# Optimization experiments

Measured on AMD Instinct MI355X. Metric: run time of the kernel, lower is better.

## Reference

```python
import jax, jax.numpy as jnp
import numpy as np

B, N, D = 4, 2048, 512
NUM_HEADS = 8
NUM_LAYERS = 2
HID_AW = D // NUM_HEADS  # 64, hidden/bottleneck of atten_weight MLP
LN_EPS = 1e-5


def _gelu(x):
    return jax.nn.gelu(x, approximate=False)


def _ln(x, g, b):
    m = jnp.mean(x, axis=-1, keepdims=True)
    v = jnp.var(x, axis=-1, keepdims=True)
    return (x - m) * jax.lax.rsqrt(v + LN_EPS) * g + b


def _mlp(x, params):
    # params: list of (W, b); gelu between layers, no act on the last layer
    for W, b in params[:-1]:
        x = _gelu(x @ W.T + b)
    W, b = params[-1]
    return x @ W.T + b


def _mha(x, valid, Wqkv, bqkv, Wo, bo):
    # x: [B, S, D], valid: [B, S] bool key mask (True = attend)
    Bx, S, Dm = x.shape
    Hd = Dm // NUM_HEADS
    qkv = x @ Wqkv.T + bqkv                      # [B, S, 3D]
    q, k, v = jnp.split(qkv, 3, axis=-1)
    def heads(t):
        return t.reshape(Bx, S, NUM_HEADS, Hd).transpose(0, 2, 1, 3)
    q, k, v = heads(q), heads(k), heads(v)       # [B, H, S, Hd]
    scores = jnp.einsum('bhqd,bhkd->bhqk', q, k) / jnp.sqrt(jnp.asarray(Hd, x.dtype))
    scores = jnp.where(valid[:, None, None, :], scores, jnp.asarray(-1e9, x.dtype))
    attn = jax.nn.softmax(scores, axis=-1)
    out = jnp.einsum('bhqk,bhkd->bhqd', attn, v).transpose(0, 2, 1, 3).reshape(Bx, S, Dm)
    return out @ Wo.T + bo


def _get_atten(emb, valid, cls_token, ln_g, ln_b, mha_params):
    # emb: [B, N, D] weighted instance embeddings; valid: [B, N] group membership
    Bx = emb.shape[0]
    seq = jnp.concatenate([jnp.broadcast_to(cls_token, (Bx, 1, D)), emb], axis=1)  # [B, N+1, D]
    mask = jnp.concatenate([jnp.ones((Bx, 1), bool), valid], axis=1)               # cls always valid
    z = _ln(seq, ln_g, ln_b)
    a = z
    for p in mha_params:
        a = _mha(a, mask, *p)
        a = _ln(z + a, ln_g, ln_b)
    return a[:, 0]  # cls embedding [B, D]


def setup_inputs() -> dict:
    key = jax.random.key(0)
    ks = jax.random.split(key, 32)
    i = iter(range(32))
    def w(shape, scale=0.02):
        return (jax.random.normal(ks[next(i)], shape, jnp.float32) * scale)
    inp = {}
    inp['x'] = jax.random.normal(ks[next(i)], (B, N, D), jnp.float32)
    inp['cls_token'] = w((1, D), 1.0)
    inp['ln_g'] = jnp.ones((D,), jnp.float32)
    inp['ln_b'] = jnp.zeros((D,), jnp.float32)
    # atten_weight MLP: D -> 64 -> 64 -> 1
    inp['aw_W0'] = w((HID_AW, D)); inp['aw_b0'] = jnp.zeros((HID_AW,), jnp.float32)
    inp['aw_W1'] = w((HID_AW, HID_AW)); inp['aw_b1'] = jnp.zeros((HID_AW,), jnp.float32)
    inp['aw_W2'] = w((1, HID_AW)); inp['aw_b2'] = jnp.zeros((1,), jnp.float32)
    # proj MLP: 2D -> D -> D -> D
    inp['pr_W0'] = w((D, 2 * D)); inp['pr_b0'] = jnp.zeros((D,), jnp.float32)
    inp['pr_W1'] = w((D, D)); inp['pr_b1'] = jnp.zeros((D,), jnp.float32)
    inp['pr_W2'] = w((D, D)); inp['pr_b2'] = jnp.zeros((D,), jnp.float32)
    # 2 shared MultiheadAttention layers
    inp['m0_Wqkv'] = w((3 * D, D)); inp['m0_bqkv'] = jnp.zeros((3 * D,), jnp.float32)
    inp['m0_Wo'] = w((D, D)); inp['m0_bo'] = jnp.zeros((D,), jnp.float32)
    inp['m1_Wqkv'] = w((3 * D, D)); inp['m1_bqkv'] = jnp.zeros((3 * D,), jnp.float32)
    inp['m1_Wo'] = w((D, D)); inp['m1_bo'] = jnp.zeros((D,), jnp.float32)
    return inp


def reference(x, cls_token, ln_g, ln_b,
              aw_W0, aw_b0, aw_W1, aw_b1, aw_W2, aw_b2,
              pr_W0, pr_b0, pr_W1, pr_b1, pr_W2, pr_b2,
              m0_Wqkv, m0_bqkv, m0_Wo, m0_bo,
              m1_Wqkv, m1_bqkv, m1_Wo, m1_bo):
    aw = [(aw_W0, aw_b0), (aw_W1, aw_b1), (aw_W2, aw_b2)]
    pr = [(pr_W0, pr_b0), (pr_W1, pr_b1), (pr_W2, pr_b2)]
    mha_params = [(m0_Wqkv, m0_bqkv, m0_Wo, m0_bo), (m1_Wqkv, m1_bqkv, m1_Wo, m1_bo)]
    # per-instance attention weights
    weight = jax.nn.sigmoid(_mlp(x, aw)[..., 0])       # [B, N]
    neg_mask = weight < 0.5
    pos_mask = jnp.logical_not(neg_mask)
    neg_emb = x * jnp.power(weight, 1.5)[..., None]    # w^(3/2)
    pos_emb = x * jnp.power(weight, 2.0 / 3.0)[..., None]  # w^(2/3)
    neg_cls = _get_atten(neg_emb, neg_mask, cls_token, ln_g, ln_b, mha_params)  # [B, D]
    pos_cls = _get_atten(pos_emb, pos_mask, cls_token, ln_g, ln_b, mha_params)  # [B, D]
    emb = jnp.concatenate([neg_cls, pos_cls], axis=-1)  # [B, 2D]
    return _mlp(emb, pr)                                # [B, D]
```

## Files before the change

kernel.cpp:

```cpp
#include <hip/hip_runtime.h>
#include <hip/hip_bf16.h>

#define B_SZ 4
#define N_INST 2048
#define D_MODEL 512
#define S_TOT 2049
#define NH 8
#define HD 64
#define VB 8
#define VROWS (VB*S_TOT)
#define NCHUNK 16

typedef __attribute__((ext_vector_type(4))) float f32x4;
typedef __attribute__((ext_vector_type(8))) short bf16x8;

__device__ __forceinline__ float gelu_exact(float x){ return 0.5f*x*(1.f+erff(x*0.70710678118654752f)); }
__device__ __forceinline__ unsigned short f2bf(float x){
  unsigned int u = __float_as_uint(x);
  u += 0x7fffu + ((u>>16)&1u);
  return (unsigned short)(u>>16);
}
__device__ __forceinline__ float bfval(unsigned short u){ return __uint_as_float(((unsigned int)u)<<16); }
__device__ __forceinline__ unsigned int pk2(unsigned short lo, unsigned short hi){
  return (unsigned int)lo | ((unsigned int)hi << 16);
}
__device__ __forceinline__ unsigned short ext16(unsigned int u, int hi){
  return (unsigned short)(hi ? (u>>16) : (u & 0xffffu));
}

#define GLOAD16(gp, lp) __builtin_amdgcn_global_load_lds( \
    (const __attribute__((address_space(1))) void*)(gp), \
    (__attribute__((address_space(3))) void*)(lp), 16, 0, 0)

__global__ __launch_bounds__(256) void transpose_w0_kernel(
    const float* __restrict__ W0, float* __restrict__ W0T) {
  int i = blockIdx.x*256 + threadIdx.x;
  if (i < 64*512){
    int h = i >> 9, k = i & 511;
    W0T[k*64 + h] = W0[i];
  }
}

__global__ __launch_bounds__(64) void aw_weight_kernel(
    const float* __restrict__ x,
    const float* __restrict__ W0T, const float* __restrict__ b0,
    const float* __restrict__ W1, const float* __restrict__ b1,
    const float* __restrict__ W2, const float* __restrict__ b2,
    float* __restrict__ weight) {
  int inst = blockIdx.x;
  int h = threadIdx.x;
  __shared__ float xs[512];
  __shared__ float hs[64];
  const float* xp = x + (size_t)inst*D_MODEL;
  for (int i=h;i<512;i+=64) xs[i] = xp[i];
  __syncthreads();
  float acc = b0[h];
  const float* w0c = W0T + h;
  #pragma unroll 16
  for (int k=0;k<512;k++)
    acc = fmaf(xs[k], w0c[k*64], acc);
  hs[h] = gelu_exact(acc);
  __syncthreads();
  const float4* w1 = (const float4*)(W1 + (size_t)h*64);
  float acc2 = b1[h];
  #pragma unroll
  for (int k4=0;k4<16;k4++){
    float4 u = w1[k4]; int k = k4*4;
    acc2 += hs[k+0]*u.x + hs[k+1]*u.y + hs[k+2]*u.z + hs[k+3]*u.w;
  }
  float h2 = gelu_exact(acc2);
  float p = h2 * W2[h];
  #pragma unroll
  for (int o=32;o;o>>=1) p += __shfl_down(p, o);
  if (h==0){
    float s = p + b2[0];
    weight[inst] = 1.f/(1.f+expf(-s));
  }
}

__global__ __launch_bounds__(256) void split_kernel(
    const float* __restrict__ w, unsigned short* __restrict__ hi,
    unsigned short* __restrict__ lo, int n) {
  int i = blockIdx.x*256 + threadIdx.x;
  if (i < n){
    float v = w[i];
    unsigned short h = f2bf(v);
    hi[i] = h;
    lo[i] = f2bf(v - bfval(h));
  }
}

__global__ __launch_bounds__(256) void compact_kernel(
    const float* __restrict__ weight,
    int* __restrict__ idx, int* __restrict__ cnt) {
  int vb = blockIdx.x;
  int b = vb & 3, branch = vb >> 2;
  int t = threadIdx.x;
  int lane = t & 63, wv = t >> 6;
  __shared__ int wsum[4];
  __shared__ int base_s;
  if (t==0){ idx[vb*S_TOT] = 0; base_s = 1; }
  __syncthreads();
  for (int c0=0; c0<N_INST; c0+=256){
    int n = c0 + t;
    float w = weight[b*N_INST + n];
    bool neg = (w < 0.5f);
    bool val = (branch==0) ? neg : !neg;
    unsigned long long m = __ballot(val);
    int prefix = __popcll(m & ((1ull<<lane)-1ull));
    if (lane==0) wsum[wv] = __popcll(m);
    __syncthreads();
    int wbase = 0;
    #pragma unroll
    for (int i=0;i<4;i++) if (i<wv) wbase += wsum[i];
    int total = wsum[0]+wsum[1]+wsum[2]+wsum[3];
    int mybase = base_s;
    if (val) idx[vb*S_TOT + mybase + wbase + prefix] = n + 1;
    __syncthreads();
    if (t==0) base_s += total;
    __syncthreads();
  }
  if (t==0) cnt[vb] = base_s;
}

__global__ __launch_bounds__(256) void build_z_kernel(
    const float* __restrict__ x, const float* __restrict__ weight,
    const float* __restrict__ cls, const float* __restrict__ g, const float* __restrict__ be,
    const int* __restrict__ idx, const int* __restrict__ cnt,
    unsigned short* __restrict__ Zh, unsigned short* __restrict__ Zl) {
  int row = blockIdx.x;
  int vb = row / S_TOT, slot = row % S_TOT;
  if (slot >= cnt[vb]) return;
  int b = vb & 3, branch = vb >> 2;
  int t = threadIdx.x;
  __shared__ float v[512];
  __shared__ float red[16];
  int pos = idx[vb*S_TOT + slot];
  float scale = 1.f;
  const float* src = cls;
  if (pos != 0){
    float w = weight[b*N_INST + (pos-1)];
    scale = (branch==0) ? powf(w, 1.5f) : powf(w, 2.0f/3.0f);
    src = x + ((size_t)b*N_INST + (pos-1))*D_MODEL;
  }
  float s1=0.f, s2=0.f;
  for (int i=t;i<512;i+=256){
    float val = src[i];
    if (pos != 0) val *= scale;
    v[i]=val; s1+=val; s2+=val*val;
  }
  __syncthreads();
  #pragma unroll
  for (int o=32;o;o>>=1){ s1+=__shfl_down(s1,o); s2+=__shfl_down(s2,o); }
  if ((t&63)==0){ red[t>>6]=s1; red[8+(t>>6)]=s2; }
  __syncthreads();
  s1 = red[0]+red[1]+red[2]+red[3];
  s2 = red[8]+red[9]+red[10]+red[11];
  float mean = s1 * (1.f/512.f);
  float var  = s2 * (1.f/512.f) - mean*mean;
  float rn = rsqrtf(var + 1e-5f);
  size_t ro = (size_t)row*512;
  for (int i=t;i<512;i+=256){
    float o = (v[i]-mean)*rn*g[i] + be[i];
    unsigned short hbits = f2bf(o);
    Zh[ro+i] = hbits;
    Zl[ro+i] = f2bf(o - bfval(hbits));
  }
}

__global__ __launch_bounds__(256) void add_ln_kernel(
    const unsigned short* __restrict__ Zh, const unsigned short* __restrict__ Zl,
    const float* __restrict__ T2,
    const float* __restrict__ g, const float* __restrict__ be,
    const int* __restrict__ cnt,
    unsigned short* __restrict__ Ah, unsigned short* __restrict__ Al) {
  int row = blockIdx.x;
  if ((row % S_TOT) >= cnt[row / S_TOT]) return;
  int t = threadIdx.x;
  __shared__ float v[512];
  __shared__ float red[16];
  size_t ro = (size_t)row*512;
  float s1=0.f, s2=0.f;
  for (int i=t;i<512;i+=256){
    float val = bfval(Zh[ro+i]) + bfval(Zl[ro+i]) + T2[ro+i];
    v[i]=val; s1+=val; s2+=val*val;
  }
  __syncthreads();
  #pragma unroll
  for (int o=32;o;o>>=1){ s1+=__shfl_down(s1,o); s2+=__shfl_down(s2,o); }
  if ((t&63)==0){ red[t>>6]=s1; red[8+(t>>6)]=s2; }
  __syncthreads();
  s1 = red[0]+red[1]+red[2]+red[3];
  s2 = red[8]+red[9]+red[10]+red[11];
  float mean = s1 * (1.f/512.f);
  float var  = s2 * (1.f/512.f) - mean*mean;
  float rn = rsqrtf(var + 1e-5f);
  for (int i=t;i<512;i+=256){
    float o = (v[i]-mean)*rn*g[i] + be[i];
    unsigned short hbits = f2bf(o);
    Ah[ro+i] = hbits;
    Al[ro+i] = f2bf(o - bfval(hbits));
  }
}

__global__ __launch_bounds__(256) void mfma_gemm_kernel(
    const unsigned short* __restrict__ Ahg, const unsigned short* __restrict__ Alg,
    const unsigned short* __restrict__ Whg, const unsigned short* __restrict__ Wlg,
    const float* __restrict__ bias, void* __restrict__ Cout,
    int M, int N, const int* __restrict__ cnt, int obf16) {
  int t = threadIdx.x;
  int bm = blockIdx.y*64, bn = blockIdx.x*64;
  {
    int r = bm + (t>>2);
    bool ok = (r < M) && ((r % S_TOT) < cnt[r / S_TOT]);
    if (__syncthreads_or(ok ? 1 : 0) == 0) return;
  }
  __shared__ unsigned short Ahs[64*64], Als[64*64], Whs[64*64], Wls[64*64];
  int lane = t & 63, w = t >> 6;
  int l15 = lane & 15, l4 = lane >> 4;

  const unsigned short* src;
  unsigned short* dst;
  if      (w == 0){ src = Ahg; dst = Ahs; }
  else if (w == 1){ src = Alg; dst = Als; }
  else if (w == 2){ src = Whg; dst = Whs; }
  else            { src = Wlg; dst = Wls; }
  int tb  = (w < 2) ? bm : bn;
  int lim = (w < 2) ? M  : N;
  int lrow = lane >> 3;
  int lg   = lane & 7;
  const unsigned short* gp[8];
  #pragma unroll
  for (int i=0;i<8;i++){
    int row_l = i*8 + lrow;
    int rg = tb + row_l; if (rg >= lim) rg = lim-1;
    gp[i] = src + (size_t)rg*512 + (size_t)((lg ^ (row_l&7))*8);
  }

  f32x4 acc[4];
  #pragma unroll
  for (int mt=0;mt<4;mt++) acc[mt] = (f32x4){0.f,0.f,0.f,0.f};

  for (int ch=0; ch<8; ch++){
    __syncthreads();
    #pragma unroll
    for (int i=0;i<8;i++)
      GLOAD16(gp[i] + ch*64, dst + i*512);
    __syncthreads();
    #pragma unroll
    for (int ks=0; ks<2; ks++){
      int wrow = w*16 + l15;
      int wgs = (ks*4 + l4) ^ (wrow & 7);
      bf16x8 wh = *(const bf16x8*)&Whs[wrow*64 + wgs*8];
      bf16x8 wl = *(const bf16x8*)&Wls[wrow*64 + wgs*8];
      #pragma unroll
      for (int mt=0;mt<4;mt++){
        int arow = mt*16 + l15;
        int ags = (ks*4 + l4) ^ (arow & 7);
        bf16x8 ah = *(const bf16x8*)&Ahs[arow*64 + ags*8];
        bf16x8 al = *(const bf16x8*)&Als[arow*64 + ags*8];
        acc[mt] = __builtin_amdgcn_mfma_f32_16x16x32_bf16(ah, wh, acc[mt], 0,0,0);
        acc[mt] = __builtin_amdgcn_mfma_f32_16x16x32_bf16(ah, wl, acc[mt], 0,0,0);
        acc[mt] = __builtin_amdgcn_mfma_f32_16x16x32_bf16(al, wh, acc[mt], 0,0,0);
      }
    }
  }
  int ncol = bn + w*16 + l15;
  float bv = bias[ncol];
  #pragma unroll
  for (int mt=0;mt<4;mt++){
    #pragma unroll
    for (int r=0;r<4;r++){
      int mrow = bm + mt*16 + l4*4 + r;
      bool ok = (mrow < M) && ((mrow % S_TOT) < cnt[mrow / S_TOT]);
      if (ok){
        float v = acc[mt][r] + bv;
        if (obf16) ((unsigned short*)Cout)[(size_t)mrow*N + ncol] = f2bf(v);
        else       ((float*)Cout)[(size_t)mrow*N + ncol] = v;
      }
    }
  }
}

__global__ __launch_bounds__(256) void flash_attn_kernel(
    const unsigned short* __restrict__ qkv, const int* __restrict__ cnt,
    unsigned short* __restrict__ Oh, unsigned short* __restrict__ Ol) {
  int vb = blockIdx.z, h = blockIdx.y;
  int cb = cnt[vb];
  int S0 = blockIdx.x * 64;
  if (S0 >= cb) return;
  int t = threadIdx.x;
  int lane = t & 63, w = t >> 6;
  int l15 = lane & 15, l4 = lane >> 4;

  __shared__ unsigned short Kbf[64*64];
  __shared__ unsigned short Vt[64*64];
  __shared__ unsigned short Pbuf[4][16*64];

  const unsigned short* basep = qkv + (size_t)(vb*S_TOT)*1536;

  int qg = S0 + w*16 + l15;
  int qr = (qg < cb) ? qg : 0;
  const unsigned short* qp = basep + (size_t)qr*1536 + h*64;
  bf16x8 Qf[2];
  Qf[0] = *(const bf16x8*)(qp + l4*8);
  Qf[1] = *(const bf16x8*)(qp + 32 + l4*8);

  float m_run = -1e30f, l_run = 0.f;
  f32x4 accO[4];
  #pragma unroll
  for (int mt=0;mt<4;mt++) accO[mt] = (f32x4){0.f,0.f,0.f,0.f};

  unsigned int* Ku = (unsigned int*)Kbf;
  unsigned int* Vu = (unsigned int*)Vt;
  const int nt = (cb + 63)/64;
  for (int kt=0; kt<nt; kt++){
    int K0 = kt*64;
    __syncthreads();
    {
      int key = t>>2;
      int keyr = (K0+key < cb) ? (K0+key) : 0;
      const unsigned short* kp = basep + (size_t)keyr*1536 + 512 + h*64 + (t&3)*16;
      uint4 a  = *(const uint4*)(kp);
      uint4 b2 = *(const uint4*)(kp+8);
      int g0 = (t&3)*2;
      int gs0 = g0 ^ (key&7), gs1 = (g0+1) ^ (key&7);
      *(uint4*)(Ku + key*32 + gs0*4) = a;
      *(uint4*)(Ku + key*32 + gs1*4) = b2;
    }
    {
      int kp2 = t & 31;
      int d8 = t >> 5;
      int k0g = K0 + 2*kp2;
      int kr0 = (k0g   < cb) ? k0g   : 0;
      int kr1 = (k0g+1 < cb) ? k0g+1 : 0;
      const unsigned short* vp0 = basep + (size_t)kr0*1536 + 1024 + h*64 + d8*8;
      const unsigned short* vp1 = basep + (size_t)kr1*1536 + 1024 + h*64 + d8*8;
      uint4 a = *(const uint4*)(vp0);
      uint4 c = *(const uint4*)(vp1);
      unsigned int au[4] = {a.x,a.y,a.z,a.w};
      unsigned int cu[4] = {c.x,c.y,c.z,c.w};
      int k8 = kp2 >> 2;
      #pragma unroll
      for (int dd=0; dd<8; dd++){
        int d = d8*8 + dd;
        Vu[d*32 + (k8 ^ (d&7))*4 + (kp2&3)] =
            pk2(ext16(au[dd>>1], dd&1), ext16(cu[dd>>1], dd&1));
      }
    }
    __syncthreads();

    f32x4 acc[4];
    #pragma unroll
    for (int mt=0;mt<4;mt++) acc[mt] = (f32x4){0.f,0.f,0.f,0.f};
    #pragma unroll
    for (int mt=0;mt<4;mt++){
      int row = mt*16 + l15;
      #pragma unroll
      for (int c=0;c<2;c++){
        int gs = (c*4 + l4) ^ (row & 7);
        bf16x8 kf = *(const bf16x8*)&Kbf[row*64 + gs*8];
        acc[mt] = __builtin_amdgcn_mfma_f32_16x16x32_bf16(kf, Qf[c], acc[mt], 0,0,0);
      }
    }
    float p[4][4];
    float tmax = -1e30f;
    #pragma unroll
    for (int mt=0;mt<4;mt++)
      #pragma unroll
      for (int r=0;r<4;r++){
        int key = K0 + mt*16 + l4*4 + r;
        float s = (key < cb) ? acc[mt][r]*0.125f : -1e30f;
        p[mt][r] = s;
        tmax = fmaxf(tmax, s);
      }
    tmax = fmaxf(tmax, __shfl_xor(tmax, 16));
    tmax = fmaxf(tmax, __shfl_xor(tmax, 32));
    float m_new = fmaxf(m_run, tmax);
    float alpha = __expf(m_run - m_new);
    float psum = 0.f;
    #pragma unroll
    for (int mt=0;mt<4;mt++)
      #pragma unroll
      for (int r=0;r<4;r++){
        float pv = __expf(p[mt][r] - m_new);
        p[mt][r] = pv; psum += pv;
      }
    psum += __shfl_xor(psum, 16);
    psum += __shfl_xor(psum, 32);
    l_run = l_run*alpha + psum;
    m_run = m_new;

    #pragma unroll
    for (int mt=0;mt<4;mt++){
      int keyl = mt*16 + l4*4;
      int gs = (keyl >> 3) ^ (l15 & 7);
      uint2 w2;
      w2.x = pk2(f2bf(p[mt][0]), f2bf(p[mt][1]));
      w2.y = pk2(f2bf(p[mt][2]), f2bf(p[mt][3]));
      *(uint2*)&Pbuf[w][ l15*64 + gs*8 + (keyl & 7) ] = w2;
    }
    #pragma unroll
    for (int mt=0;mt<4;mt++){
      accO[mt][0]*=alpha; accO[mt][1]*=alpha; accO[mt][2]*=alpha; accO[mt][3]*=alpha;
    }
    #pragma unroll
    for (int c2=0;c2<2;c2++){
      int gpv = (c2*4 + l4) ^ (l15 & 7);
      bf16x8 pf = *(const bf16x8*)&Pbuf[w][ l15*64 + gpv*8 ];
      #pragma unroll
      for (int mt=0;mt<4;mt++){
        int d = mt*16 + l15;
        int gv = (c2*4 + l4) ^ (d & 7);
        bf16x8 vf = *(const bf16x8*)&Vt[ d*64 + gv*8 ];
        accO[mt] = __builtin_amdgcn_mfma_f32_16x16x32_bf16(vf, pf, accO[mt], 0,0,0);
      }
    }
  }
  if (qg < cb){
    float inv = 1.f/l_run;
    size_t ro = ((size_t)(vb*S_TOT) + qg)*512 + h*64;
    #pragma unroll
    for (int mt=0;mt<4;mt++){
      float v0 = accO[mt][0]*inv, v1 = accO[mt][1]*inv;
      float v2 = accO[mt][2]*inv, v3 = accO[mt][3]*inv;
      unsigned short h0=f2bf(v0), h1=f2bf(v1), h2=f2bf(v2), h3=f2bf(v3);
      uint2 hw; hw.x = pk2(h0,h1); hw.y = pk2(h2,h3);
      uint2 lw;
      lw.x = pk2(f2bf(v0-bfval(h0)), f2bf(v1-bfval(h1)));
      lw.y = pk2(f2bf(v2-bfval(h2)), f2bf(v3-bfval(h3)));
      *(uint2*)&Oh[ro + mt*16 + l4*4] = hw;
      *(uint2*)&Ol[ro + mt*16 + l4*4] = lw;
    }
  }
}

__global__ __launch_bounds__(256) void row0_q_kernel(
    const unsigned short* __restrict__ Ah, const unsigned short* __restrict__ Al,
    const float* __restrict__ Wq, const float* __restrict__ bq,
    float* __restrict__ q0) {
  int vb = blockIdx.y;
  int n = blockIdx.x*4 + (threadIdx.x >> 6);
  int lane = threadIdx.x & 63;
  __shared__ float xs[512];
  size_t ro = (size_t)(vb*S_TOT)*512;
  for (int i=threadIdx.x; i<512; i+=256)
    xs[i] = bfval(Ah[ro+i]) + bfval(Al[ro+i]);
  __syncthreads();
  const float* wr = Wq + (size_t)n*512;
  float acc = 0.f;
  #pragma unroll
  for (int k=lane*4; k<512; k+=256){
    float4 u = *(const float4*)(wr + k);
    acc += xs[k]*u.x + xs[k+1]*u.y + xs[k+2]*u.z + xs[k+3]*u.w;
  }
  #pragma unroll
  for (int o=32;o;o>>=1) acc += __shfl_down(acc, o);
  if (lane==0) q0[vb*512 + n] = acc + bq[n];
}

__global__ __launch_bounds__(256) void attn_row0_part_kernel(
    const unsigned short* __restrict__ kv, const float* __restrict__ q0,
    const int* __restrict__ cnt,
    float* __restrict__ partM, float* __restrict__ partL,
    float* __restrict__ partN) {
  int h = blockIdx.x, vb = blockIdx.y, c = blockIdx.z;
  int cb = cnt[vb];
  int chunk = (cb + NCHUNK-1)/NCHUNK;
  int j0 = c*chunk;
  int j1 = j0+chunk; if (j1 > cb) j1 = cb;
  int t = threadIdx.x;
  int pidx = (vb*NH + h)*NCHUNK + c;
  __shared__ float qs[64];
  __shared__ float sc[144];
  __shared__ float red[8];
  __shared__ float redO[4][64];
  if (t < 64) qs[t] = q0[vb*512 + h*64 + t]*0.125f;
  __syncthreads();
  if (j0 >= cb){
    if (t == 0){ partM[pidx] = -1e30f; partL[pidx] = 0.f; }
    if (t < 64) partN[(size_t)pidx*64 + t] = 0.f;
    return;
  }
  const unsigned short* base = kv + (size_t)vb*S_TOT*1024;
  int len = j1 - j0;
  float lmax = -1e30f;
  for (int jj=t; jj<len; jj+=256){
    const unsigned short* kp = base + (size_t)(j0+jj)*1024 + h*64;
    float s = 0.f;
    #pragma unroll
    for (int d8=0; d8<8; d8++){
      uint4 a = *(const uint4*)(kp + d8*8);
      unsigned int au[4] = {a.x,a.y,a.z,a.w};
      #pragma unroll
      for (int q2=0; q2<4; q2++){
        s += qs[d8*8+q2*2]*bfval(ext16(au[q2],0))
           + qs[d8*8+q2*2+1]*bfval(ext16(au[q2],1));
      }
    }
    sc[jj] = s;
    lmax = fmaxf(lmax, s);
  }
  #pragma unroll
  for (int o=32;o;o>>=1) lmax = fmaxf(lmax, __shfl_down(lmax,o));
  if ((t&63)==0) red[t>>6] = lmax;
  __syncthreads();
  float m = fmaxf(fmaxf(red[0],red[1]),fmaxf(red[2],red[3]));
  float lsum = 0.f;
  for (int jj=t; jj<len; jj+=256){
    float p = __expf(sc[jj]-m);
    sc[jj] = p; lsum += p;
  }
  #pragma unroll
  for (int o=32;o;o>>=1) lsum += __shfl_down(lsum,o);
  __syncthreads();
  if ((t&63)==0) red[t>>6] = lsum;
  __syncthreads();
  float l = red[0]+red[1]+red[2]+red[3];
  int d = t & 63, rr = t >> 6;
  float acc = 0.f;
  for (int jj=rr; jj<len; jj+=4)
    acc += sc[jj]*bfval(base[(size_t)(j0+jj)*1024 + 512 + h*64 + d]);
  redO[rr][d] = acc;
  __syncthreads();
  if (t < 64){
    partN[(size_t)pidx*64 + t] = redO[0][t]+redO[1][t]+redO[2][t]+redO[3][t];
    if (t==0){ partM[pidx] = m; partL[pidx] = l; }
  }
}

__global__ __launch_bounds__(64) void attn_row0_combine_kernel(
    const float* __restrict__ partM, const float* __restrict__ partL,
    const float* __restrict__ partN, float* __restrict__ out0) {
  int h = blockIdx.x, vb = blockIdx.y;
  int t = threadIdx.x;
  int pb = (vb*NH + h)*NCHUNK;
  float m = -1e30f;
  #pragma unroll
  for (int c=0;c<NCHUNK;c++) m = fmaxf(m, partM[pb+c]);
  float lsum = 0.f, nsum = 0.f;
  #pragma unroll
  for (int c=0;c<NCHUNK;c++){
    float w = __expf(partM[pb+c]-m);
    lsum += w*partL[pb+c];
    nsum += w*partN[(size_t)(pb+c)*64 + t];
  }
  out0[vb*512 + h*64 + t] = nsum/lsum;
}

__global__ __launch_bounds__(256) void row0_proj_ln_kernel(
    const float* __restrict__ attn0, const float* __restrict__ Wo, const float* __restrict__ bo,
    const unsigned short* __restrict__ Zh, const unsigned short* __restrict__ Zl,
    const float* __restrict__ g, const float* __restrict__ be,
    float* __restrict__ clsbuf) {
  int vb = blockIdx.x, t = threadIdx.x;
  int b = vb & 3, branch = vb >> 2;
  __shared__ float xin[512];
  __shared__ float y[512];
  __shared__ float red[16];
  for (int i=t;i<512;i+=256) xin[i] = attn0[vb*512+i];
  __syncthreads();
  size_t z0 = (size_t)vb*S_TOT*512;
  for (int n=t;n<512;n+=256){
    const float4* wr = (const float4*)(Wo + (size_t)n*512);
    float acc = bo[n];
    for (int k4=0;k4<128;k4++){
      float4 u = wr[k4]; int k=k4*4;
      acc += xin[k+0]*u.x + xin[k+1]*u.y + xin[k+2]*u.z + xin[k+3]*u.w;
    }
    y[n] = acc + bfval(Zh[z0+n]) + bfval(Zl[z0+n]);
  }
  __syncthreads();
  float s1=0.f, s2=0.f;
  for (int i=t;i<512;i+=256){ float a=y[i]; s1+=a; s2+=a*a; }
  #pragma unroll
  for (int o=32;o;o>>=1){ s1+=__shfl_down(s1,o); s2+=__shfl_down(s2,o); }
  if ((t&63)==0){ red[t>>6]=s1; red[8+(t>>6)]=s2; }
  __syncthreads();
  s1 = red[0]+red[1]+red[2]+red[3];
  s2 = red[8]+red[9]+red[10]+red[11];
  float mean = s1*(1.f/512.f);
  float var  = s2*(1.f/512.f) - mean*mean;
  float rn = rsqrtf(var + 1e-5f);
  for (int i=t;i<512;i+=256)
    clsbuf[b*1024 + branch*512 + i] = (y[i]-mean)*rn*g[i] + be[i];
}

__global__ __launch_bounds__(256) void fm_layer_kernel(
    const float* __restrict__ in, const float* __restrict__ W,
    const float* __restrict__ bias, float* __restrict__ out,
    int K, int N, int act) {
  int b = blockIdx.y;
  int n = blockIdx.x*4 + (threadIdx.x >> 6);
  int lane = threadIdx.x & 63;
  __shared__ float xs[1024];
  for (int i=threadIdx.x; i<K; i+=256) xs[i] = in[(size_t)b*K + i];
  __syncthreads();
  const float* wr = W + (size_t)n*K;
  float acc = 0.f;
  #pragma unroll 4
  for (int k=lane*4; k<K; k+=256){
    float4 u = *(const float4*)(wr + k);
    acc += xs[k]*u.x + xs[k+1]*u.y + xs[k+2]*u.z + xs[k+3]*u.w;
  }
  #pragma unroll
  for (int o=32;o;o>>=1) acc += __shfl_down(acc, o);
  if (lane==0){
    float v = acc + bias[n];
    if (act) v = gelu_exact(v);
    out[(size_t)b*N + n] = v;
  }
}

extern "C" void kernel_launch(void* const* d_in, const int* in_sizes, int n_in,
                              void* d_out, int out_size, void* d_ws, size_t ws_size,
                              hipStream_t stream) {
  const float* x      = (const float*)d_in[0];
  const float* cls_tk = (const float*)d_in[1];
  const float* ln_g   = (const float*)d_in[2];
  const float* ln_b   = (const float*)d_in[3];
  const float* aw_W0  = (const float*)d_in[4];  const float* aw_b0 = (const float*)d_in[5];
  const float* aw_W1  = (const float*)d_in[6];  const float* aw_b1 = (const float*)d_in[7];
  const float* aw_W2  = (const float*)d_in[8];  const float* aw_b2 = (const float*)d_in[9];
  const float* pr_W0  = (const float*)d_in[10]; const float* pr_b0 = (const float*)d_in[11];
  const float* pr_W1  = (const float*)d_in[12]; const float* pr_b1 = (const float*)d_in[13];
  const float* pr_W2  = (const float*)d_in[14]; const float* pr_b2 = (const float*)d_in[15];
  const float* mWqkv[2] = {(const float*)d_in[16], (const float*)d_in[20]};
  const float* mbqkv[2] = {(const float*)d_in[17], (const float*)d_in[21]};
  const float* mWo[2]   = {(const float*)d_in[18], (const float*)d_in[22]};
  const float* mbo[2]   = {(const float*)d_in[19], (const float*)d_in[23]};

  float* ws = (float*)d_ws;
  size_t off = 0;
  float* weight = ws + off; off += 8192;
  int*   idx    = (int*)(ws + off); off += VROWS + 8;
  int*   cnt    = (int*)(ws + off); off += 16;
  float* W0T    = ws + off; off += 32768;
  const size_t HBUF = (size_t)VROWS*512/2;
  unsigned short* Zh = (unsigned short*)(ws + off); off += HBUF;
  unsigned short* Zl = (unsigned short*)(ws + off); off += HBUF;
  float* QKVr   = ws + off; off += (size_t)VROWS*1536/2;
  unsigned short* QKVb = (unsigned short*)QKVr;
  float* T2     = QKVr;
  unsigned short* KVb  = (unsigned short*)QKVr;
  unsigned short* Oh = (unsigned short*)(ws + off); off += HBUF;
  unsigned short* Ol = (unsigned short*)(ws + off); off += HBUF;
  unsigned short* Wq0h = (unsigned short*)(ws + off); off += 393216;
  unsigned short* Wq0l = (unsigned short*)(ws + off); off += 393216;
  unsigned short* Wq1h = (unsigned short*)(ws + off); off += 393216;
  unsigned short* Wq1l = (unsigned short*)(ws + off); off += 393216;
  unsigned short* Wo0h = (unsigned short*)(ws + off); off += 131072;
  unsigned short* Wo0l = (unsigned short*)(ws + off); off += 131072;
  float* attn0  = ws + off; off += VB*512;
  float* q0buf  = ws + off; off += VB*512;
  float* clsb   = ws + off; off += 4096;
  float* h1buf  = ws + off; off += 2048;
  float* h2buf  = ws + off; off += 2048;
  float* partM  = ws + off; off += VB*NH*NCHUNK;
  float* partL  = ws + off; off += VB*NH*NCHUNK;
  float* partN  = ws + off; off += (size_t)VB*NH*NCHUNK*64;
  (void)ws_size; (void)in_sizes; (void)n_in; (void)out_size;

  transpose_w0_kernel<<<(32768+255)/256, 256, 0, stream>>>(aw_W0, W0T);
  aw_weight_kernel<<<B_SZ*N_INST, 64, 0, stream>>>(
      x, W0T, aw_b0, aw_W1, aw_b1, aw_W2, aw_b2, weight);

  split_kernel<<<(786432+255)/256, 256, 0, stream>>>(mWqkv[0], Wq0h, Wq0l, 786432);
  split_kernel<<<(786432+255)/256, 256, 0, stream>>>(mWqkv[1], Wq1h, Wq1l, 786432);
  split_kernel<<<(262144+255)/256, 256, 0, stream>>>(mWo[0],  Wo0h, Wo0l, 262144);

  const int MT = (VROWS + 63)/64;
  compact_kernel<<<VB, 256, 0, stream>>>(weight, idx, cnt);
  build_z_kernel<<<VROWS, 256, 0, stream>>>(x, weight, cls_tk, ln_g, ln_b, idx, cnt, Zh, Zl);
  mfma_gemm_kernel<<<dim3(1536/64, MT), 256, 0, stream>>>(
      Zh, Zl, Wq0h, Wq0l, mbqkv[0], QKVb, VROWS, 1536, cnt, 1);
  flash_attn_kernel<<<dim3((S_TOT+63)/64, NH, VB), 256, 0, stream>>>(QKVb, cnt, Oh, Ol);
  mfma_gemm_kernel<<<dim3(512/64, MT), 256, 0, stream>>>(
      Oh, Ol, Wo0h, Wo0l, mbo[0], T2, VROWS, 512, cnt, 0);
  add_ln_kernel<<<VROWS, 256, 0, stream>>>(Zh, Zl, T2, ln_g, ln_b, cnt, Oh, Ol);
  row0_q_kernel<<<dim3(128, VB), 256, 0, stream>>>(Oh, Ol, mWqkv[1], mbqkv[1], q0buf);
  mfma_gemm_kernel<<<dim3(1024/64, MT), 256, 0, stream>>>(
      Oh, Ol, Wq1h + (size_t)512*512, Wq1l + (size_t)512*512,
      mbqkv[1] + 512, KVb, VROWS, 1024, cnt, 1);
  attn_row0_part_kernel<<<dim3(NH, VB, NCHUNK), 256, 0, stream>>>(
      KVb, q0buf, cnt, partM, partL, partN);
  attn_row0_combine_kernel<<<dim3(NH, VB), 64, 0, stream>>>(
      partM, partL, partN, attn0);
  row0_proj_ln_kernel<<<VB, 256, 0, stream>>>(
      attn0, mWo[1], mbo[1], Zh, Zl, ln_g, ln_b, clsb);
  fm_layer_kernel<<<dim3(128, B_SZ), 256, 0, stream>>>(clsb,  pr_W0, pr_b0, h1buf, 1024, 512, 1);
  fm_layer_kernel<<<dim3(128, B_SZ), 256, 0, stream>>>(h1buf, pr_W1, pr_b1, h2buf,  512, 512, 1);
  fm_layer_kernel<<<dim3(128, B_SZ), 256, 0, stream>>>(h2buf, pr_W2, pr_b2, (float*)d_out, 512, 512, 0);
}
```

Measured before the change: 486.4 us.

## Process two query fragments per wave in flash attention to reuse K/V tiles

Each flash attention block now covers 128 query rows instead of 64, with each wave handling two 16-row query fragments that share the same K and V tiles staged in shared memory. The aim is to halve the global K/V loads and LDS staging per query row and the number of barrier rounds. In exchange it uses more registers for a second set of accumulators and softmax state, and launches half as many blocks, which can lower occupancy and parallelism across the device.

```diff
diff --git a/kernel.cpp b/kernel.cpp
--- a/kernel.cpp
+++ b/kernel.cpp
@@ -287,7 +287,7 @@
     unsigned short* __restrict__ Oh, unsigned short* __restrict__ Ol) {
   int vb = blockIdx.z, h = blockIdx.y;
   int cb = cnt[vb];
-  int S0 = blockIdx.x * 64;
+  int S0 = blockIdx.x * 128;
   if (S0 >= cb) return;
   int t = threadIdx.x;
   int lane = t & 63, w = t >> 6;
@@ -299,17 +299,23 @@
 
   const unsigned short* basep = qkv + (size_t)(vb*S_TOT)*1536;
 
-  int qg = S0 + w*16 + l15;
-  int qr = (qg < cb) ? qg : 0;
-  const unsigned short* qp = basep + (size_t)qr*1536 + h*64;
-  bf16x8 Qf[2];
-  Qf[0] = *(const bf16x8*)(qp + l4*8);
-  Qf[1] = *(const bf16x8*)(qp + 32 + l4*8);
-
-  float m_run = -1e30f, l_run = 0.f;
-  f32x4 accO[4];
-  #pragma unroll
-  for (int mt=0;mt<4;mt++) accO[mt] = (f32x4){0.f,0.f,0.f,0.f};
+  int qg[2];
+  bf16x8 Qf[2][2];
+  #pragma unroll
+  for (int qf=0; qf<2; qf++){
+    qg[qf] = S0 + w*32 + qf*16 + l15;
+    int qr = (qg[qf] < cb) ? qg[qf] : 0;
+    const unsigned short* qp = basep + (size_t)qr*1536 + h*64;
+    Qf[qf][0] = *(const bf16x8*)(qp + l4*8);
+    Qf[qf][1] = *(const bf16x8*)(qp + 32 + l4*8);
+  }
+
+  float m_run[2] = {-1e30f, -1e30f}, l_run[2] = {0.f, 0.f};
+  f32x4 accO[2][4];
+  #pragma unroll
+  for (int qf=0;qf<2;qf++)
+    #pragma unroll
+    for (int mt=0;mt<4;mt++) accO[qf][mt] = (f32x4){0.f,0.f,0.f,0.f};
 
   unsigned int* Ku = (unsigned int*)Kbf;
   unsigned int* Vu = (unsigned int*)Vt;
@@ -350,87 +356,94 @@
     }
     __syncthreads();
 
-    f32x4 acc[4];
     #pragma unroll
-    for (int mt=0;mt<4;mt++) acc[mt] = (f32x4){0.f,0.f,0.f,0.f};
-    #pragma unroll
-    for (int mt=0;mt<4;mt++){
-      int row = mt*16 + l15;
-      #pragma unroll
-      for (int c=0;c<2;c++){
-        int gs = (c*4 + l4) ^ (row & 7);
-        bf16x8 kf = *(const bf16x8*)&Kbf[row*64 + gs*8];
-        acc[mt] = __builtin_amdgcn_mfma_f32_16x16x32_bf16(kf, Qf[c], acc[mt], 0,0,0);
+    for (int qf=0; qf<2; qf++){
+      f32x4 acc[4];
+      #pragma unroll
+      for (int mt=0;mt<4;mt++) acc[mt] = (f32x4){0.f,0.f,0.f,0.f};
+      #pragma unroll
+      for (int mt=0;mt<4;mt++){
+        int row = mt*16 + l15;
+        #pragma unroll
+        for (int c=0;c<2;c++){
+          int gs = (c*4 + l4) ^ (row & 7);
+          bf16x8 kf = *(const bf16x8*)&Kbf[row*64 + gs*8];
+          acc[mt] = __builtin_amdgcn_mfma_f32_16x16x32_bf16(kf, Qf[qf][c], acc[mt], 0,0,0);
+        }
+      }
+      float p[4][4];
+      float tmax = -1e30f;
+      #pragma unroll
+      for (int mt=0;mt<4;mt++)
+        #pragma unroll
+        for (int r=0;r<4;r++){
+          int key = K0 + mt*16 + l4*4 + r;
+          float s = (key < cb) ? acc[mt][r]*0.125f : -1e30f;
+          p[mt][r] = s;
+          tmax = fmaxf(tmax, s);
+        }
+      tmax = fmaxf(tmax, __shfl_xor(tmax, 16));
+      tmax = fmaxf(tmax, __shfl_xor(tmax, 32));
+      float m_new = fmaxf(m_run[qf], tmax);
+      float alpha = __expf(m_run[qf] - m_new);
+      float psum = 0.f;
+      #pragma unroll
+      for (int mt=0;mt<4;mt++)
+        #pragma unroll
+        for (int r=0;r<4;r++){
+          float pv = __expf(p[mt][r] - m_new);
+          p[mt][r] = pv; psum += pv;
+        }
+      psum += __shfl_xor(psum, 16);
+      psum += __shfl_xor(psum, 32);
+      l_run[qf] = l_run[qf]*alpha + psum;
+      m_run[qf] = m_new;
+
+      #pragma unroll
+      for (int mt=0;mt<4;mt++){
+        int keyl = mt*16 + l4*4;
+        int gs = (keyl >> 3) ^ (l15 & 7);
+        uint2 w2;
+        w2.x = pk2(f2bf(p[mt][0]), f2bf(p[mt][1]));
+        w2.y = pk2(f2bf(p[mt][2]), f2bf(p[mt][3]));
+        *(uint2*)&Pbuf[w][ l15*64 + gs*8 + (keyl & 7) ] = w2;
+      }
+      #pragma unroll
+      for (int mt=0;mt<4;mt++){
+        accO[qf][mt][0]*=alpha; accO[qf][mt][1]*=alpha;
+        accO[qf][mt][2]*=alpha; accO[qf][mt][3]*=alpha;
+      }
+      #pragma unroll
+      for (int c2=0;c2<2;c2++){
+        int gpv = (c2*4 + l4) ^ (l15 & 7);
+        bf16x8 pf = *(const bf16x8*)&Pbuf[w][ l15*64 + gpv*8 ];
+        #pragma unroll
+        for (int mt=0;mt<4;mt++){
+          int d = mt*16 + l15;
+          int gv = (c2*4 + l4) ^ (d & 7);
+          bf16x8 vf = *(const bf16x8*)&Vt[ d*64 + gv*8 ];
+          accO[qf][mt] = __builtin_amdgcn_mfma_f32_16x16x32_bf16(vf, pf, accO[qf][mt], 0,0,0);
+        }
       }
     }
-    float p[4][4];
-    float tmax = -1e30f;
-    #pragma unroll
-    for (int mt=0;mt<4;mt++)
-      #pragma unroll
-      for (int r=0;r<4;r++){
-        int key = K0 + mt*16 + l4*4 + r;
-        float s = (key < cb) ? acc[mt][r]*0.125f : -1e30f;
-        p[mt][r] = s;
-        tmax = fmaxf(tmax, s);
-      }
-    tmax = fmaxf(tmax, __shfl_xor(tmax, 16));
-    tmax = fmaxf(tmax, __shfl_xor(tmax, 32));
-    float m_new = fmaxf(m_run, tmax);
-    float alpha = __expf(m_run - m_new);
-    float psum = 0.f;
-    #pragma unroll
-    for (int mt=0;mt<4;mt++)
-      #pragma unroll
-      for (int r=0;r<4;r++){
-        float pv = __expf(p[mt][r] - m_new);
-        p[mt][r] = pv; psum += pv;
-      }
-    psum += __shfl_xor(psum, 16);
-    psum += __shfl_xor(psum, 32);
-    l_run = l_run*alpha + psum;
-    m_run = m_new;
-
-    #pragma unroll
-    for (int mt=0;mt<4;mt++){
-      int keyl = mt*16 + l4*4;
-      int gs = (keyl >> 3) ^ (l15 & 7);
-      uint2 w2;
-      w2.x = pk2(f2bf(p[mt][0]), f2bf(p[mt][1]));
-      w2.y = pk2(f2bf(p[mt][2]), f2bf(p[mt][3]));
-      *(uint2*)&Pbuf[w][ l15*64 + gs*8 + (keyl & 7) ] = w2;
-    }
-    #pragma unroll
-    for (int mt=0;mt<4;mt++){
-      accO[mt][0]*=alpha; accO[mt][1]*=alpha; accO[mt][2]*=alpha; accO[mt][3]*=alpha;
-    }
-    #pragma unroll
-    for (int c2=0;c2<2;c2++){
-      int gpv = (c2*4 + l4) ^ (l15 & 7);
-      bf16x8 pf = *(const bf16x8*)&Pbuf[w][ l15*64 + gpv*8 ];
+  }
+  #pragma unroll
+  for (int qf=0; qf<2; qf++){
+    if (qg[qf] < cb){
+      float inv = 1.f/l_run[qf];
+      size_t ro = ((size_t)(vb*S_TOT) + qg[qf])*512 + h*64;
       #pragma unroll
       for (int mt=0;mt<4;mt++){
-        int d = mt*16 + l15;
-        int gv = (c2*4 + l4) ^ (d & 7);
-        bf16x8 vf = *(const bf16x8*)&Vt[ d*64 + gv*8 ];
-        accO[mt] = __builtin_amdgcn_mfma_f32_16x16x32_bf16(vf, pf, accO[mt], 0,0,0);
-      }
-    }
-  }
-  if (qg < cb){
-    float inv = 1.f/l_run;
-    size_t ro = ((size_t)(vb*S_TOT) + qg)*512 + h*64;
-    #pragma unroll
-    for (int mt=0;mt<4;mt++){
-      float v0 = accO[mt][0]*inv, v1 = accO[mt][1]*inv;
-      float v2 = accO[mt][2]*inv, v3 = accO[mt][3]*inv;
-      unsigned short h0=f2bf(v0), h1=f2bf(v1), h2=f2bf(v2), h3=f2bf(v3);
-      uint2 hw; hw.x = pk2(h0,h1); hw.y = pk2(h2,h3);
-      uint2 lw;
-      lw.x = pk2(f2bf(v0-bfval(h0)), f2bf(v1-bfval(h1)));
-      lw.y = pk2(f2bf(v2-bfval(h2)), f2bf(v3-bfval(h3)));
-      *(uint2*)&Oh[ro + mt*16 + l4*4] = hw;
-      *(uint2*)&Ol[ro + mt*16 + l4*4] = lw;
+        float v0 = accO[qf][mt][0]*inv, v1 = accO[qf][mt][1]*inv;
+        float v2 = accO[qf][mt][2]*inv, v3 = accO[qf][mt][3]*inv;
+        unsigned short h0=f2bf(v0), h1=f2bf(v1), h2=f2bf(v2), h3=f2bf(v3);
+        uint2 hw; hw.x = pk2(h0,h1); hw.y = pk2(h2,h3);
+        uint2 lw;
+        lw.x = pk2(f2bf(v0-bfval(h0)), f2bf(v1-bfval(h1)));
+        lw.y = pk2(f2bf(v2-bfval(h2)), f2bf(v3-bfval(h3)));
+        *(uint2*)&Oh[ro + mt*16 + l4*4] = hw;
+        *(uint2*)&Ol[ro + mt*16 + l4*4] = lw;
+      }
     }
   }
 }
@@ -674,7 +687,7 @@
   build_z_kernel<<<VROWS, 256, 0, stream>>>(x, weight, cls_tk, ln_g, ln_b, idx, cnt, Zh, Zl);
   mfma_gemm_kernel<<<dim3(1536/64, MT), 256, 0, stream>>>(
       Zh, Zl, Wq0h, Wq0l, mbqkv[0], QKVb, VROWS, 1536, cnt, 1);
-  flash_attn_kernel<<<dim3((S_TOT+63)/64, NH, VB), 256, 0, stream>>>(QKVb, cnt, Oh, Ol);
+  flash_attn_kernel<<<dim3((S_TOT+127)/128, NH, VB), 256, 0, stream>>>(QKVb, cnt, Oh, Ol);
   mfma_gemm_kernel<<<dim3(512/64, MT), 256, 0, stream>>>(
       Oh, Ol, Wo0h, Wo0l, mbo[0], T2, VROWS, 512, cnt, 0);
   add_ln_kernel<<<VROWS, 256, 0, stream>>>(Zh, Zl, T2, ln_g, ln_b, cnt, Oh, Ol);
```

New measurement: 467.1 us. 4.0% less time.
